# Optimization experiments

Measured on AMD Instinct MI355X. Metric: run time of the kernel, lower is better.

Reference implementation:

```python
import jax, jax.numpy as jnp
import numpy as np

N, E, IN_DIM, HID, G, NCLS, LAYERS = 200000, 1200000, 128, 64, 1024, 6, 3
BN_EPS = 1e-5


def _bn(x, g, b, m, v):
    # eval-mode BatchNorm1d with running stats
    return (x - m) * jax.lax.rsqrt(v + BN_EPS) * g + b


def setup_inputs() -> dict:
    key = jax.random.key(0)
    ks = jax.random.split(key, 24)
    s = 0.05
    d = {
        "x": jax.random.normal(ks[0], (N, IN_DIM), jnp.float32),
        "edge_index": jax.random.randint(ks[1], (2, E), 0, N, dtype=jnp.int32),
        "batch": jnp.sort(jax.random.randint(ks[2], (N,), 0, G, dtype=jnp.int32)),
        # input embedding + input BN
        "emb_w": jax.random.normal(ks[3], (IN_DIM, HID), jnp.float32) * s,
        "emb_b": jnp.zeros((HID,), jnp.float32),
        "ibn_g": jnp.ones((HID,), jnp.float32),
        "ibn_b": jnp.zeros((HID,), jnp.float32),
        "ibn_m": jax.random.normal(ks[4], (HID,), jnp.float32) * 0.1,
        "ibn_v": jax.random.uniform(ks[5], (HID,), jnp.float32, 0.5, 1.5),
        # stacked per-layer GIN MLP params [LAYERS, ...]
        "fc1_w": jax.random.normal(ks[6], (LAYERS, HID, HID), jnp.float32) * s,
        "fc1_b": jnp.zeros((LAYERS, HID), jnp.float32),
        "mbn_g": jnp.ones((LAYERS, HID), jnp.float32),
        "mbn_b": jnp.zeros((LAYERS, HID), jnp.float32),
        "mbn_m": jax.random.normal(ks[7], (LAYERS, HID), jnp.float32) * 0.1,
        "mbn_v": jax.random.uniform(ks[8], (LAYERS, HID), jnp.float32, 0.5, 1.5),
        "fc2_w": jax.random.normal(ks[9], (LAYERS, HID, HID), jnp.float32) * s,
        "fc2_b": jnp.zeros((LAYERS, HID), jnp.float32),
        # stacked per-layer outer BN params
        "obn_g": jnp.ones((LAYERS, HID), jnp.float32),
        "obn_b": jnp.zeros((LAYERS, HID), jnp.float32),
        "obn_m": jax.random.normal(ks[10], (LAYERS, HID), jnp.float32) * 0.1,
        "obn_v": jax.random.uniform(ks[11], (LAYERS, HID), jnp.float32, 0.5, 1.5),
        # classifier head
        "cls1_w": jax.random.normal(ks[12], (HID, HID // 2), jnp.float32) * s,
        "cls1_b": jnp.zeros((HID // 2,), jnp.float32),
        "cls2_w": jax.random.normal(ks[13], (HID // 2, NCLS), jnp.float32) * s,
        "cls2_b": jnp.zeros((NCLS,), jnp.float32),
    }
    return d


def reference(x, edge_index, batch,
              emb_w, emb_b, ibn_g, ibn_b, ibn_m, ibn_v,
              fc1_w, fc1_b, mbn_g, mbn_b, mbn_m, mbn_v, fc2_w, fc2_b,
              obn_g, obn_b, obn_m, obn_v,
              cls1_w, cls1_b, cls2_w, cls2_b):
    n = x.shape[0]
    src, dst = edge_index[0], edge_index[1]

    # input embed -> BN -> relu (dropout = identity in eval)
    h = jnp.dot(x, emb_w) + emb_b
    h = jax.nn.relu(_bn(h, ibn_g, ibn_b, ibn_m, ibn_v))

    for i in range(LAYERS):
        # GINConv (eps=0): aggregate neighbors via scatter-add, then MLP
        agg = jax.ops.segment_sum(h[src], dst, num_segments=n)
        z = h + agg
        z = jnp.dot(z, fc1_w[i]) + fc1_b[i]
        z = jax.nn.relu(_bn(z, mbn_g[i], mbn_b[i], mbn_m[i], mbn_v[i]))
        z = jnp.dot(z, fc2_w[i]) + fc2_b[i]
        # outer BN + relu
        h = jax.nn.relu(_bn(z, obn_g[i], obn_b[i], obn_m[i], obn_v[i]))

    # global mean pool per graph
    sums = jax.ops.segment_sum(h, batch, num_segments=G)
    cnts = jax.ops.segment_sum(jnp.ones((n,), h.dtype), batch, num_segments=G)
    pooled = sums / jnp.maximum(cnts, 1.0)[:, None]

    # classifier
    out = jax.nn.relu(jnp.dot(pooled, cls1_w) + cls1_b)
    out = jnp.dot(out, cls2_w) + cls2_b
    return out
```

## Files before the change

### kernel.cpp

```cpp
#include <hip/hip_runtime.h>
#include <hip/hip_bf16.h>

#define N_NODES 200000
#define N_EDGES 1200000
#define IN_DIM  128
#define HID     64
#define NGRAPH  1024
#define NCLS    6
#define BN_EPS  1e-5f

#define TILE_N   64
#define ZS       68
#define ECAP     1024

#define SCAN_CHUNK 1024
#define NBLK_SCAN ((N_NODES + SCAN_CHUNK - 1) / SCAN_CHUNK)

#define NBKT   128
#define BRANGE 1568
#define BCAP   12288
#define EPB    4096
#define NB_BIN ((N_EDGES + EPB - 1) / EPB)

#define SWZ(s) ((s) ^ (((s) >> 4) & 3))

typedef short bf16x8 __attribute__((ext_vector_type(8)));
typedef float f32x4  __attribute__((ext_vector_type(4)));
#define MFMA16(a,b,c) __builtin_amdgcn_mfma_f32_16x16x32_bf16((a),(b),(c),0,0,0)

template<bool V> struct BoolC { static constexpr bool value = V; };

__device__ __forceinline__ unsigned short f2bf(float f) {
    union { __hip_bfloat16 h; unsigned short u; } v; v.h = __float2bfloat16(f); return v.u;
}
__device__ __forceinline__ float bfbits2f(unsigned short u) {
    union { unsigned int i; float f; } v; v.i = ((unsigned int)u) << 16; return v.f;
}
__device__ __forceinline__ void cvt4(const f32x4& x, uint2& hi, uint2& lo) {
    const unsigned short h0 = f2bf(x[0]), h1 = f2bf(x[1]), h2 = f2bf(x[2]), h3 = f2bf(x[3]);
    hi.x = (unsigned)h0 | ((unsigned)h1 << 16);
    hi.y = (unsigned)h2 | ((unsigned)h3 << 16);
    const unsigned short l0 = f2bf(x[0] - bfbits2f(h0)), l1 = f2bf(x[1] - bfbits2f(h1));
    const unsigned short l2 = f2bf(x[2] - bfbits2f(h2)), l3 = f2bf(x[3] - bfbits2f(h3));
    lo.x = (unsigned)l0 | ((unsigned)l1 << 16);
    lo.y = (unsigned)l2 | ((unsigned)l3 << 16);
}

__global__ __launch_bounds__(256) void setup_kernel(
    const float* __restrict__ emb_w, unsigned short* __restrict__ wpe,
    const float* __restrict__ fc1, const float* __restrict__ fc2,
    unsigned short* __restrict__ wpf,
    const int* __restrict__ batch, int* __restrict__ goffs,
    int* __restrict__ gcnt)
{
    const int b = blockIdx.x, t = threadIdx.x;
    if (b < 64) {
        const int idx = b * 256 + t;
        const int j = idx & 7, l = (idx >> 3) & 63;
        const int plane = (idx >> 9) & 1, s = (idx >> 10) & 3, ct = (idx >> 12) & 3;
        const int n = ct * 16 + (l & 15);
        const int k = s * 32 + (l >> 4) * 8 + j;
        const float f = emb_w[k * 64 + n];
        const unsigned short hb = f2bf(f);
        wpe[idx] = plane ? f2bf(f - bfbits2f(hb)) : hb;
    } else if (b < 256) {
        const int idx = (b - 64) * 256 + t;
        const int j = idx & 7, l = (idx >> 3) & 63;
        const int plane = (idx >> 9) & 1, s = (idx >> 10) & 1, ct = (idx >> 11) & 3;
        const int g = (idx >> 13) & 1, layer = idx >> 14;
        const int n = ct * 16 + (l & 15);
        const int k = s * 32 + (l >> 4) * 8 + j;
        const float* W = g ? fc2 : fc1;
        const float f = W[(layer * 64 + k) * 64 + n];
        const unsigned short hb = f2bf(f);
        wpf[idx] = plane ? f2bf(f - bfbits2f(hb)) : hb;
    } else {
        if (b == 256 && t < NBKT) gcnt[t] = 0;
        const int g = (b - 256) * 256 + t;
        if (g > NGRAPH) return;
        if (g == NGRAPH) { goffs[NGRAPH] = N_NODES; return; }
        int lo = 0, hi = N_NODES;
        while (lo < hi) {
            const int mid = (lo + hi) >> 1;
            if (batch[mid] < g) lo = mid + 1; else hi = mid;
        }
        goffs[g] = lo;
    }
}

__global__ __launch_bounds__(256) void bin_kernel(
    const int* __restrict__ src, const int* __restrict__ dst,
    int* __restrict__ gcnt, unsigned* __restrict__ ebin)
{
    __shared__ int hist[NBKT];
    __shared__ int basis[NBKT];
    const int t = threadIdx.x;
    const int base = blockIdx.x * EPB;
    if (t < NBKT) hist[t] = 0;
    __syncthreads();
    int sv[16], dv[16];
    #pragma unroll
    for (int i = 0; i < 16; i++) {
        const int e = base + t + i * 256;
        if (e < N_EDGES) {
            sv[i] = __builtin_nontemporal_load(&src[e]);
            dv[i] = __builtin_nontemporal_load(&dst[e]);
            atomicAdd(&hist[dv[i] / BRANGE], 1);
        } else { sv[i] = -1; dv[i] = -1; }
    }
    __syncthreads();
    if (t < NBKT) { basis[t] = atomicAdd(&gcnt[t], hist[t]); hist[t] = 0; }
    __syncthreads();
    #pragma unroll
    for (int i = 0; i < 16; i++) {
        if (dv[i] >= 0) {
            const int bb = dv[i] / BRANGE;
            const int dl = dv[i] - bb * BRANGE;
            const int pos = basis[bb] + atomicAdd(&hist[bb], 1);
            __builtin_nontemporal_store(
                (unsigned)sv[i] | ((unsigned)dl << 18),
                &ebin[(size_t)bb * BCAP + pos]);
        }
    }
}

__global__ __launch_bounds__(512) void bindeg_kernel(
    const int* __restrict__ gcnt, const unsigned* __restrict__ ebin,
    int* __restrict__ deg)
{
    __shared__ int hist[BRANGE];
    const int b = blockIdx.x, t = threadIdx.x;
    for (int i = t; i < BRANGE; i += 512) hist[i] = 0;
    __syncthreads();
    const int cnt = gcnt[b];
    const int r0 = b * BRANGE;
    const unsigned* __restrict__ eb = ebin + (size_t)b * BCAP;
    for (int i = t; i < cnt; i += 512) {
        const unsigned e = __builtin_nontemporal_load(&eb[i]);
        atomicAdd(&hist[e >> 18], 1);
    }
    __syncthreads();
    for (int i = t; i < BRANGE; i += 512)
        if (r0 + i < N_NODES) deg[r0 + i] = hist[i];
}

__global__ __launch_bounds__(512) void binscatter_kernel(
    const int* __restrict__ gcnt, const unsigned* __restrict__ ebin,
    const int* __restrict__ offs, int* __restrict__ csr_src)
{
    __shared__ int cur[BRANGE];
    const int b = blockIdx.x, t = threadIdx.x;
    const int r0 = b * BRANGE;
    const int lim = (r0 + BRANGE <= N_NODES) ? BRANGE : (N_NODES - r0);
    for (int i = t; i < lim; i += 512) cur[i] = offs[r0 + i];
    __syncthreads();
    const int cnt = gcnt[b];
    const unsigned* __restrict__ eb = ebin + (size_t)b * BCAP;
    for (int i = t; i < cnt; i += 512) {
        const unsigned e = __builtin_nontemporal_load(&eb[i]);
        const int pos = atomicAdd(&cur[e >> 18], 1);
        csr_src[pos] = (int)(e & 0x3FFFFu);
    }
}

__global__ __launch_bounds__(256) void scan_sum_kernel(
    const int* __restrict__ deg, int* __restrict__ bsum)
{
    __shared__ int sd[256];
    const int b = blockIdx.x, t = threadIdx.x;
    const int base = b * SCAN_CHUNK;
    int s = 0;
    #pragma unroll
    for (int i = 0; i < SCAN_CHUNK / 256; i++) {
        const int idx = base + t + i * 256;
        s += (idx < N_NODES) ? deg[idx] : 0;
    }
    sd[t] = s; __syncthreads();
    for (int off = 128; off > 0; off >>= 1) {
        if (t < off) sd[t] += sd[t + off];
        __syncthreads();
    }
    if (t == 0) bsum[b] = sd[0];
}

__global__ __launch_bounds__(256) void scan_block_kernel(
    const int* __restrict__ bsum, int* __restrict__ boff, int* __restrict__ offs)
{
    __shared__ int sd[256];
    const int t = threadIdx.x;
    const int v = (t < NBLK_SCAN) ? bsum[t] : 0;
    sd[t] = v; __syncthreads();
    for (int off = 1; off < 256; off <<= 1) {
        const int u = (t >= off) ? sd[t - off] : 0;
        __syncthreads();
        sd[t] += u;
        __syncthreads();
    }
    if (t < NBLK_SCAN) boff[t] = sd[t] - v;
    if (t == 0) offs[N_NODES] = N_EDGES;
}

__global__ __launch_bounds__(256) void scan_scatter_kernel(
    const int* __restrict__ deg, const int* __restrict__ boff, int* __restrict__ offs)
{
    __shared__ int sd[256];
    const int b = blockIdx.x, t = threadIdx.x;
    const int base = b * SCAN_CHUNK + t * 4;
    int d0 = 0, d1 = 0, d2 = 0, d3 = 0;
    if (base + 0 < N_NODES) d0 = deg[base + 0];
    if (base + 1 < N_NODES) d1 = deg[base + 1];
    if (base + 2 < N_NODES) d2 = deg[base + 2];
    if (base + 3 < N_NODES) d3 = deg[base + 3];
    const int ts = d0 + d1 + d2 + d3;
    sd[t] = ts; __syncthreads();
    for (int off = 1; off < 256; off <<= 1) {
        const int u = (t >= off) ? sd[t - off] : 0;
        __syncthreads();
        sd[t] += u;
        __syncthreads();
    }
    const int excl = sd[t] - ts + boff[b];
    if (base + 0 < N_NODES) offs[base + 0] = excl;
    if (base + 1 < N_NODES) offs[base + 1] = excl + d0;
    if (base + 2 < N_NODES) offs[base + 2] = excl + d0 + d1;
    if (base + 3 < N_NODES) offs[base + 3] = excl + d0 + d1 + d2;
}

__global__ __launch_bounds__(256) void pool_kernel(
    const float* __restrict__ h, const int* __restrict__ goffs,
    float* __restrict__ pooled, float* __restrict__ cnt)
{
    __shared__ f32x4 red[4][16];
    const int g = blockIdx.x, t = threadIdx.x;
    const int s = goffs[g], e = goffs[g + 1];
    const int grp = t >> 4;
    const int q = t & 15;
    f32x4 acc = {0.f, 0.f, 0.f, 0.f};
    for (int n = s + grp; n < e; n += 16) {
        const f32x4 v = __builtin_nontemporal_load(
            (const f32x4*)(h + (size_t)n * HID + q * 4));
        acc += v;
    }
    #pragma unroll
    for (int off = 16; off <= 32; off <<= 1) {
        acc[0] += __shfl_xor(acc[0], off, 64);
        acc[1] += __shfl_xor(acc[1], off, 64);
        acc[2] += __shfl_xor(acc[2], off, 64);
        acc[3] += __shfl_xor(acc[3], off, 64);
    }
    const int wv = t >> 6, lane = t & 63;
    if (lane < 16) red[wv][lane] = acc;
    __syncthreads();
    if (t < 16) {
        f32x4 a = red[0][t] + red[1][t] + red[2][t] + red[3][t];
        *(f32x4*)(pooled + (size_t)g * HID + t * 4) = a;
    }
    if (t == 0) cnt[g] = (float)(e - s);
}

__global__ __launch_bounds__(256) void embed_kernel(
    const float* __restrict__ x, const unsigned short* __restrict__ wpe,
    const float* __restrict__ bias,
    const float* __restrict__ bn_g, const float* __restrict__ bn_b,
    const float* __restrict__ bn_m, const float* __restrict__ bn_v,
    float* __restrict__ h)
{
    __shared__ __align__(16) float Ush[8192];
    __shared__ float BNs[128];
    short* Abuf = (short*)Ush;
    float* Ztmp = Ush;
    const int t = threadIdx.x, lane = t & 63, w = t >> 6;
    const int base = blockIdx.x * TILE_N;

    if (t < 64) {
        const float s = bn_g[t] * rsqrtf(bn_v[t] + BN_EPS);
        BNs[t] = s;
        BNs[64 + t] = bias[t] * s + bn_b[t] - bn_m[t] * s;
    }
    #pragma unroll
    for (int i = 0; i < 8; i++) {
        const int idx = t + i * 256;
        const int n = idx >> 5, k4 = idx & 31;
        const f32x4 v = __builtin_nontemporal_load(
            (const f32x4*)(x + (size_t)(base + n) * IN_DIM + k4 * 4));
        uint2 hi, lo; cvt4(v, hi, lo);
        const int s = k4 >> 3, lc = (n & 15) + 16 * ((k4 >> 1) & 3);
        const int half = k4 & 1, wm = n >> 4;
        const int sl0 = ((wm * 4 + s) * 2 + 0) * 64 + lc;
        const int sl1 = ((wm * 4 + s) * 2 + 1) * 64 + lc;
        *(uint2*)&Abuf[SWZ(sl0) * 8 + half * 4] = hi;
        *(uint2*)&Abuf[SWZ(sl1) * 8 + half * 4] = lo;
    }
    __syncthreads();

    const bf16x8* A = (const bf16x8*)Abuf;
    const bf16x8* B = (const bf16x8*)wpe;
    bf16x8 ah[4], al[4];
    #pragma unroll
    for (int s = 0; s < 4; s++) {
        ah[s] = A[SWZ(((w * 4 + s) * 2 + 0) * 64 + lane)];
        al[s] = A[SWZ(((w * 4 + s) * 2 + 1) * 64 + lane)];
    }
    __syncthreads();
    const int q = lane >> 4, c = lane & 15;
    #pragma unroll
    for (int ct = 0; ct < 4; ct++) {
        f32x4 acc = {0.f, 0.f, 0.f, 0.f};
        #pragma unroll
        for (int s = 0; s < 4; s++) {
            const bf16x8 bh = B[(ct << 9) + (s << 7) + lane];
            const bf16x8 bl = B[(ct << 9) + (s << 7) + 64 + lane];
            acc = MFMA16(ah[s], bh, acc);
            acc = MFMA16(ah[s], bl, acc);
            acc = MFMA16(al[s], bh, acc);
        }
        const int n = ct * 16 + c;
        const float sc = BNs[n], sh = BNs[64 + n];
        #pragma unroll
        for (int r = 0; r < 4; r++)
            Ztmp[(w * 16 + q * 4 + r) * ZS + n] = fmaxf(acc[r] * sc + sh, 0.f);
    }
    __syncthreads();
    #pragma unroll
    for (int i = 0; i < 4; i++) {
        const int idx = t + i * 256, n = idx >> 4, k4 = idx & 15;
        *(f32x4*)(h + (size_t)(base + n) * HID + k4 * 4) =
            *(const f32x4*)(&Ztmp[n * ZS + k4 * 4]);
    }
}

__global__ __launch_bounds__(256, 7) void agg_mlp_kernel(
    const float* __restrict__ hin, float* __restrict__ hout,
    const int* __restrict__ offs, const int* __restrict__ csr,
    const unsigned short* __restrict__ wp1, const unsigned short* __restrict__ wp2,
    const float* __restrict__ b1, const float* __restrict__ g1,
    const float* __restrict__ bb1, const float* __restrict__ m1, const float* __restrict__ v1,
    const float* __restrict__ b2, const float* __restrict__ g2,
    const float* __restrict__ bb2, const float* __restrict__ m2, const float* __restrict__ v2)
{
    __shared__ __align__(16) float Ush[TILE_N * ZS];
    __shared__ int   OF[TILE_N + 1];
    __shared__ int   EIDX[ECAP];
    __shared__ float BNs[256];
    short* Abuf = (short*)Ush;
    float* Ztmp = Ush;
    const int t = threadIdx.x, lane = t & 63, w = t >> 6;
    const int sub = lane >> 4, cq = lane & 15;
    const int base = blockIdx.x * TILE_N;

    if (t < 64) {
        const float sa = g1[t] * rsqrtf(v1[t] + BN_EPS);
        BNs[t] = sa; BNs[64 + t] = b1[t] * sa + bb1[t] - m1[t] * sa;
        const float sb = g2[t] * rsqrtf(v2[t] + BN_EPS);
        BNs[128 + t] = sb; BNs[192 + t] = b2[t] * sb + bb2[t] - m2[t] * sb;
    }
    if (t <= TILE_N) OF[t] = offs[base + t];
    const int segStart = offs[base];
    const int segEnd   = offs[base + TILE_N];
    for (int i = t; i < segEnd - segStart; i += 256)
        if (i < ECAP) EIDX[i] = csr[segStart + i];
    __syncthreads();

    const float* __restrict__ hc = hin + cq * 4;
    const bool allLds = (segEnd - segStart) <= ECAP;

    auto gather_pass = [&](auto ldsTag) {
        constexpr bool LDSONLY = decltype(ldsTag)::value;
        #pragma unroll
        for (int pp = 0; pp < 2; pp++) {
            const int mlA = (pp * 2 + 0) * 4 + sub;
            const int mlB = (pp * 2 + 1) * 4 + sub;
            const int nlA = w * 16 + mlA, nlB = w * 16 + mlB;
            int eA = OF[nlA]; const int eA1 = OF[nlA + 1];
            int eB = OF[nlB]; const int eB1 = OF[nlB + 1];
            const int eAm = (eA1 - 1 > segStart) ? eA1 - 1 : segStart;
            const int eBm = (eB1 - 1 > segStart) ? eB1 - 1 : segStart;
            f32x4 accA = *(const f32x4*)(hin + (size_t)(base + nlA) * HID + cq * 4);
            f32x4 accB = *(const f32x4*)(hin + (size_t)(base + nlB) * HID + cq * 4);
            while (eA < eA1 || eB < eB1) {
                int ia[4], ib[4];
                #pragma unroll
                for (int k = 0; k < 4; k++) {
                    const int ea = (eA + k < eAm) ? eA + k : eAm;
                    const int eb = (eB + k < eBm) ? eB + k : eBm;
                    const int la = ea - segStart, lb = eb - segStart;
                    if (LDSONLY) {
                        ia[k] = EIDX[la];
                        ib[k] = EIDX[lb];
                    } else {
                        ia[k] = (la < ECAP) ? EIDX[la] : csr[ea];
                        ib[k] = (lb < ECAP) ? EIDX[lb] : csr[eb];
                    }
                }
                f32x4 va[4], vb[4];
                #pragma unroll
                for (int k = 0; k < 4; k++) {
                    va[k] = *(const f32x4*)(hc + (size_t)ia[k] * HID);
                    vb[k] = *(const f32x4*)(hc + (size_t)ib[k] * HID);
                }
                #pragma unroll
                for (int k = 0; k < 4; k++) {
                    const float ma = (eA + k < eA1) ? 1.f : 0.f;
                    const float mb = (eB + k < eB1) ? 1.f : 0.f;
                    accA += va[k] * ma;
                    accB += vb[k] * mb;
                }
                eA += 4; eB += 4;
            }
            {
                uint2 hi, lo; cvt4(accA, hi, lo);
                const int s = cq >> 3, lc = mlA + 16 * ((cq >> 1) & 3), half = cq & 1;
                const int sl0 = ((w * 2 + s) * 2 + 0) * 64 + lc;
                const int sl1 = ((w * 2 + s) * 2 + 1) * 64 + lc;
                *(uint2*)&Abuf[SWZ(sl0) * 8 + half * 4] = hi;
                *(uint2*)&Abuf[SWZ(sl1) * 8 + half * 4] = lo;
            }
            {
                uint2 hi, lo; cvt4(accB, hi, lo);
                const int s = cq >> 3, lc = mlB + 16 * ((cq >> 1) & 3), half = cq & 1;
                const int sl0 = ((w * 2 + s) * 2 + 0) * 64 + lc;
                const int sl1 = ((w * 2 + s) * 2 + 1) * 64 + lc;
                *(uint2*)&Abuf[SWZ(sl0) * 8 + half * 4] = hi;
                *(uint2*)&Abuf[SWZ(sl1) * 8 + half * 4] = lo;
            }
        }
    };
    if (allLds) gather_pass(BoolC<true>{});
    else        gather_pass(BoolC<false>{});
    __syncthreads();

    const bf16x8* A = (const bf16x8*)Abuf;
    const int q = lane >> 4, c = lane & 15;

    {
        const bf16x8 a0h = A[SWZ(((w * 2 + 0) * 2 + 0) * 64 + lane)];
        const bf16x8 a0l = A[SWZ(((w * 2 + 0) * 2 + 1) * 64 + lane)];
        const bf16x8 a1h = A[SWZ(((w * 2 + 1) * 2 + 0) * 64 + lane)];
        const bf16x8 a1l = A[SWZ(((w * 2 + 1) * 2 + 1) * 64 + lane)];
        __syncthreads();
        const bf16x8* B = (const bf16x8*)wp1;
        #pragma unroll
        for (int ct = 0; ct < 4; ct++) {
            const bf16x8 b0h = B[(ct << 8) + lane];
            const bf16x8 b0l = B[(ct << 8) + 64 + lane];
            const bf16x8 b1h_ = B[(ct << 8) + 128 + lane];
            const bf16x8 b1l_ = B[(ct << 8) + 192 + lane];
            f32x4 acc = {0.f, 0.f, 0.f, 0.f};
            acc = MFMA16(a0h, b0h, acc);
            acc = MFMA16(a0h, b0l, acc);
            acc = MFMA16(a0l, b0h, acc);
            acc = MFMA16(a1h, b1h_, acc);
            acc = MFMA16(a1h, b1l_, acc);
            acc = MFMA16(a1l, b1h_, acc);
            const int n = ct * 16 + c;
            const float sc = BNs[n], sh = BNs[64 + n];
            #pragma unroll
            for (int r = 0; r < 4; r++)
                Ztmp[(w * 16 + q * 4 + r) * ZS + n] = fmaxf(acc[r] * sc + sh, 0.f);
        }
    }
    __syncthreads();

    {
        const int m = t >> 2;
        f32x4 vv[4];
        #pragma unroll
        for (int d = 0; d < 4; d++) {
            const int k4 = (t & 3) * 4 + d;
            vv[d] = *(const f32x4*)(&Ztmp[m * ZS + k4 * 4]);
        }
        __syncthreads();
        #pragma unroll
        for (int d = 0; d < 4; d++) {
            const int k4 = (t & 3) * 4 + d;
            uint2 hi, lo; cvt4(vv[d], hi, lo);
            const int s = k4 >> 3, lc = (m & 15) + 16 * ((k4 >> 1) & 3);
            const int half = k4 & 1, wm = m >> 4;
            const int sl0 = ((wm * 2 + s) * 2 + 0) * 64 + lc;
            const int sl1 = ((wm * 2 + s) * 2 + 1) * 64 + lc;
            *(uint2*)&Abuf[SWZ(sl0) * 8 + half * 4] = hi;
            *(uint2*)&Abuf[SWZ(sl1) * 8 + half * 4] = lo;
        }
    }
    __syncthreads();

    {
        const bf16x8 a0h = A[SWZ(((w * 2 + 0) * 2 + 0) * 64 + lane)];
        const bf16x8 a0l = A[SWZ(((w * 2 + 0) * 2 + 1) * 64 + lane)];
        const bf16x8 a1h = A[SWZ(((w * 2 + 1) * 2 + 0) * 64 + lane)];
        const bf16x8 a1l = A[SWZ(((w * 2 + 1) * 2 + 1) * 64 + lane)];
        __syncthreads();
        const bf16x8* B = (const bf16x8*)wp2;
        #pragma unroll
        for (int ct = 0; ct < 4; ct++) {
            const bf16x8 b0h = B[(ct << 8) + lane];
            const bf16x8 b0l = B[(ct << 8) + 64 + lane];
            const bf16x8 b1h_ = B[(ct << 8) + 128 + lane];
            const bf16x8 b1l_ = B[(ct << 8) + 192 + lane];
            f32x4 acc = {0.f, 0.f, 0.f, 0.f};
            acc = MFMA16(a0h, b0h, acc);
            acc = MFMA16(a0h, b0l, acc);
            acc = MFMA16(a0l, b0h, acc);
            acc = MFMA16(a1h, b1h_, acc);
            acc = MFMA16(a1h, b1l_, acc);
            acc = MFMA16(a1l, b1h_, acc);
            const int n = ct * 16 + c;
            const float sc = BNs[128 + n], sh = BNs[192 + n];
            #pragma unroll
            for (int r = 0; r < 4; r++)
                Ztmp[(w * 16 + q * 4 + r) * ZS + n] = fmaxf(acc[r] * sc + sh, 0.f);
        }
    }
    __syncthreads();

    #pragma unroll
    for (int i = 0; i < 4; i++) {
        const int idx = t + i * 256, n = idx >> 4, k4 = idx & 15;
        *(f32x4*)(hout + (size_t)(base + n) * HID + k4 * 4) =
            *(const f32x4*)(&Ztmp[n * ZS + k4 * 4]);
    }
}

__global__ __launch_bounds__(64) void cls_kernel(
    const float* __restrict__ pooled, const float* __restrict__ cnt,
    const float* __restrict__ w1, const float* __restrict__ b1,
    const float* __restrict__ w2, const float* __restrict__ b2,
    float* __restrict__ out)
{
    const int g = blockIdx.x;
    const int lane = threadIdx.x;
    const float c = cnt[g];
    const float p = pooled[(size_t)g * HID + lane] / fmaxf(c, 1.f);
    float acc = (lane < 32) ? b1[lane] : 0.f;
    #pragma unroll
    for (int k = 0; k < 64; k++) {
        const float pk = __shfl(p, k, 64);
        if (lane < 32) acc += pk * w1[k * 32 + lane];
    }
    const float hmid = fmaxf(acc, 0.f);
    float acc2 = (lane < NCLS) ? b2[lane] : 0.f;
    #pragma unroll
    for (int k = 0; k < 32; k++) {
        const float hk = __shfl(hmid, k, 64);
        if (lane < NCLS) acc2 += hk * w2[k * NCLS + lane];
    }
    if (lane < NCLS) out[(size_t)g * NCLS + lane] = acc2;
}

extern "C" void kernel_launch(void* const* d_in, const int* in_sizes, int n_in,
                              void* d_out, int out_size, void* d_ws, size_t ws_size,
                              hipStream_t stream) {
    const float* x     = (const float*)d_in[0];
    const int*   ei    = (const int*)d_in[1];
    const int*   batch = (const int*)d_in[2];
    const float* emb_w = (const float*)d_in[3];
    const float* emb_b = (const float*)d_in[4];
    const float* ibn_g = (const float*)d_in[5];
    const float* ibn_b = (const float*)d_in[6];
    const float* ibn_m = (const float*)d_in[7];
    const float* ibn_v = (const float*)d_in[8];
    const float* fc1_w = (const float*)d_in[9];
    const float* fc1_b = (const float*)d_in[10];
    const float* mbn_g = (const float*)d_in[11];
    const float* mbn_b = (const float*)d_in[12];
    const float* mbn_m = (const float*)d_in[13];
    const float* mbn_v = (const float*)d_in[14];
    const float* fc2_w = (const float*)d_in[15];
    const float* fc2_b = (const float*)d_in[16];
    const float* obn_g = (const float*)d_in[17];
    const float* obn_b = (const float*)d_in[18];
    const float* obn_m = (const float*)d_in[19];
    const float* obn_v = (const float*)d_in[20];
    const float* cls1w = (const float*)d_in[21];
    const float* cls1b = (const float*)d_in[22];
    const float* cls2w = (const float*)d_in[23];
    const float* cls2b = (const float*)d_in[24];

    float* h0     = (float*)d_ws;
    float* h1     = h0 + (size_t)N_NODES * HID;
    float* pooled = h1 + (size_t)N_NODES * HID;
    float* cnt    = pooled + NGRAPH * HID;
    int*   deg    = (int*)(cnt + NGRAPH);
    int*   offs   = deg + N_NODES;
    int*   bsum   = offs + (N_NODES + 1);
    int*   boff   = bsum + NBLK_SCAN;
    int*   csr    = boff + NBLK_SCAN;
    unsigned short* wpe = (unsigned short*)(csr + N_EDGES);
    unsigned short* wpf = wpe + 16384;
    int*   goffs  = (int*)(wpf + 49152);
    int*   gcnt   = goffs + (NGRAPH + 1);
    unsigned* ebin = (unsigned*)h0;

    const int* src = ei;
    const int* dst = ei + N_EDGES;

    setup_kernel<<<261, 256, 0, stream>>>(emb_w, wpe, fc1_w, fc2_w, wpf,
                                          batch, goffs, gcnt);

    bin_kernel<<<NB_BIN, 256, 0, stream>>>(src, dst, gcnt, ebin);
    bindeg_kernel<<<NBKT, 512, 0, stream>>>(gcnt, ebin, deg);
    scan_sum_kernel<<<NBLK_SCAN, 256, 0, stream>>>(deg, bsum);
    scan_block_kernel<<<1, 256, 0, stream>>>(bsum, boff, offs);
    scan_scatter_kernel<<<NBLK_SCAN, 256, 0, stream>>>(deg, boff, offs);
    binscatter_kernel<<<NBKT, 512, 0, stream>>>(gcnt, ebin, offs, csr);

    const int gemm_blocks = N_NODES / TILE_N;
    embed_kernel<<<gemm_blocks, 256, 0, stream>>>(x, wpe, emb_b,
                                                  ibn_g, ibn_b, ibn_m, ibn_v, h0);

    const float* hin = h0;
    float* hout = h1;
    for (int i = 0; i < 3; i++) {
        agg_mlp_kernel<<<gemm_blocks, 256, 0, stream>>>(
            hin, hout, offs, csr,
            wpf + (size_t)(i * 2 + 0) * 8192, wpf + (size_t)(i * 2 + 1) * 8192,
            fc1_b + i * HID, mbn_g + i * HID, mbn_b + i * HID, mbn_m + i * HID, mbn_v + i * HID,
            fc2_b + i * HID, obn_g + i * HID, obn_b + i * HID, obn_m + i * HID, obn_v + i * HID);
        const float* tmp = hin; hin = hout; hout = (float*)tmp;
    }

    pool_kernel<<<NGRAPH, 256, 0, stream>>>(h1, goffs, pooled, cnt);

    cls_kernel<<<NGRAPH, 64, 0, stream>>>(pooled, cnt, cls1w, cls1b, cls2w, cls2b,
                                          (float*)d_out);
}
```

Baseline: 496.2 us.

## Fuse CSR offset scan into bin-degree kernel and mean-pool into last GIN layer

Replaces the degree histogram plus three-kernel global scan with one kernel. Each bucket block builds its local histogram, scans the bucket counts to get its base, and writes CSR offsets directly. The last GIN layer now accumulates per-graph sums with atomics instead of writing h, which removes the separate pool kernel and one full h write and read. It also relaxes launch bounds occupancy from 7 to 6 and adds a memset. The trade-off is atomic contention on pooled and nondeterministic float summation order.

After: 465.7 us. 6.1% less time.

```diff
diff --git a/kernel.cpp b/kernel.cpp
--- a/kernel.cpp
+++ b/kernel.cpp
@@ -12,9 +12,6 @@
 #define TILE_N   64
 #define ZS       68
 #define ECAP     1024
-
-#define SCAN_CHUNK 1024
-#define NBLK_SCAN ((N_NODES + SCAN_CHUNK - 1) / SCAN_CHUNK)
 
 #define NBKT   128
 #define BRANGE 1568
@@ -124,24 +121,52 @@
     }
 }
 
-__global__ __launch_bounds__(512) void bindeg_kernel(
+__global__ __launch_bounds__(512) void binoffs_kernel(
     const int* __restrict__ gcnt, const unsigned* __restrict__ ebin,
-    int* __restrict__ deg)
+    int* __restrict__ offs)
 {
     __shared__ int hist[BRANGE];
+    __shared__ int bscan[NBKT];
+    __shared__ int pscan[512];
     const int b = blockIdx.x, t = threadIdx.x;
     for (int i = t; i < BRANGE; i += 512) hist[i] = 0;
+    if (t < NBKT) bscan[t] = gcnt[t];
     __syncthreads();
     const int cnt = gcnt[b];
-    const int r0 = b * BRANGE;
     const unsigned* __restrict__ eb = ebin + (size_t)b * BCAP;
     for (int i = t; i < cnt; i += 512) {
         const unsigned e = __builtin_nontemporal_load(&eb[i]);
         atomicAdd(&hist[e >> 18], 1);
     }
     __syncthreads();
-    for (int i = t; i < BRANGE; i += 512)
-        if (r0 + i < N_NODES) deg[r0 + i] = hist[i];
+    for (int off = 1; off < NBKT; off <<= 1) {
+        const int u = (t >= off && t < NBKT) ? bscan[t - off] : 0;
+        __syncthreads();
+        if (t < NBKT) bscan[t] += u;
+        __syncthreads();
+    }
+    const int bucketBase = (b == 0) ? 0 : bscan[b - 1];
+    const int i0 = t * 4;
+    const int h0v = (i0 + 0 < BRANGE) ? hist[i0 + 0] : 0;
+    const int h1v = (i0 + 1 < BRANGE) ? hist[i0 + 1] : 0;
+    const int h2v = (i0 + 2 < BRANGE) ? hist[i0 + 2] : 0;
+    const int h3v = (i0 + 3 < BRANGE) ? hist[i0 + 3] : 0;
+    const int ts = h0v + h1v + h2v + h3v;
+    pscan[t] = ts;
+    __syncthreads();
+    for (int off = 1; off < 512; off <<= 1) {
+        const int u = (t >= off) ? pscan[t - off] : 0;
+        __syncthreads();
+        pscan[t] += u;
+        __syncthreads();
+    }
+    const int excl = pscan[t] - ts + bucketBase;
+    const int r0 = b * BRANGE;
+    if (i0 + 0 < BRANGE && r0 + i0 + 0 < N_NODES) offs[r0 + i0 + 0] = excl;
+    if (i0 + 1 < BRANGE && r0 + i0 + 1 < N_NODES) offs[r0 + i0 + 1] = excl + h0v;
+    if (i0 + 2 < BRANGE && r0 + i0 + 2 < N_NODES) offs[r0 + i0 + 2] = excl + h0v + h1v;
+    if (i0 + 3 < BRANGE && r0 + i0 + 3 < N_NODES) offs[r0 + i0 + 3] = excl + h0v + h1v + h2v;
+    if (b == NBKT - 1 && t == 0) offs[N_NODES] = N_EDGES;
 }
 
 __global__ __launch_bounds__(512) void binscatter_kernel(
@@ -161,101 +186,6 @@
         const int pos = atomicAdd(&cur[e >> 18], 1);
         csr_src[pos] = (int)(e & 0x3FFFFu);
     }
-}
-
-__global__ __launch_bounds__(256) void scan_sum_kernel(
-    const int* __restrict__ deg, int* __restrict__ bsum)
-{
-    __shared__ int sd[256];
-    const int b = blockIdx.x, t = threadIdx.x;
-    const int base = b * SCAN_CHUNK;
-    int s = 0;
-    #pragma unroll
-    for (int i = 0; i < SCAN_CHUNK / 256; i++) {
-        const int idx = base + t + i * 256;
-        s += (idx < N_NODES) ? deg[idx] : 0;
-    }
-    sd[t] = s; __syncthreads();
-    for (int off = 128; off > 0; off >>= 1) {
-        if (t < off) sd[t] += sd[t + off];
-        __syncthreads();
-    }
-    if (t == 0) bsum[b] = sd[0];
-}
-
-__global__ __launch_bounds__(256) void scan_block_kernel(
-    const int* __restrict__ bsum, int* __restrict__ boff, int* __restrict__ offs)
-{
-    __shared__ int sd[256];
-    const int t = threadIdx.x;
-    const int v = (t < NBLK_SCAN) ? bsum[t] : 0;
-    sd[t] = v; __syncthreads();
-    for (int off = 1; off < 256; off <<= 1) {
-        const int u = (t >= off) ? sd[t - off] : 0;
-        __syncthreads();
-        sd[t] += u;
-        __syncthreads();
-    }
-    if (t < NBLK_SCAN) boff[t] = sd[t] - v;
-    if (t == 0) offs[N_NODES] = N_EDGES;
-}
-
-__global__ __launch_bounds__(256) void scan_scatter_kernel(
-    const int* __restrict__ deg, const int* __restrict__ boff, int* __restrict__ offs)
-{
-    __shared__ int sd[256];
-    const int b = blockIdx.x, t = threadIdx.x;
-    const int base = b * SCAN_CHUNK + t * 4;
-    int d0 = 0, d1 = 0, d2 = 0, d3 = 0;
-    if (base + 0 < N_NODES) d0 = deg[base + 0];
-    if (base + 1 < N_NODES) d1 = deg[base + 1];
-    if (base + 2 < N_NODES) d2 = deg[base + 2];
-    if (base + 3 < N_NODES) d3 = deg[base + 3];
-    const int ts = d0 + d1 + d2 + d3;
-    sd[t] = ts; __syncthreads();
-    for (int off = 1; off < 256; off <<= 1) {
-        const int u = (t >= off) ? sd[t - off] : 0;
-        __syncthreads();
-        sd[t] += u;
-        __syncthreads();
-    }
-    const int excl = sd[t] - ts + boff[b];
-    if (base + 0 < N_NODES) offs[base + 0] = excl;
-    if (base + 1 < N_NODES) offs[base + 1] = excl + d0;
-    if (base + 2 < N_NODES) offs[base + 2] = excl + d0 + d1;
-    if (base + 3 < N_NODES) offs[base + 3] = excl + d0 + d1 + d2;
-}
-
-__global__ __launch_bounds__(256) void pool_kernel(
-    const float* __restrict__ h, const int* __restrict__ goffs,
-    float* __restrict__ pooled, float* __restrict__ cnt)
-{
-    __shared__ f32x4 red[4][16];
-    const int g = blockIdx.x, t = threadIdx.x;
-    const int s = goffs[g], e = goffs[g + 1];
-    const int grp = t >> 4;
-    const int q = t & 15;
-    f32x4 acc = {0.f, 0.f, 0.f, 0.f};
-    for (int n = s + grp; n < e; n += 16) {
-        const f32x4 v = __builtin_nontemporal_load(
-            (const f32x4*)(h + (size_t)n * HID + q * 4));
-        acc += v;
-    }
-    #pragma unroll
-    for (int off = 16; off <= 32; off <<= 1) {
-        acc[0] += __shfl_xor(acc[0], off, 64);
-        acc[1] += __shfl_xor(acc[1], off, 64);
-        acc[2] += __shfl_xor(acc[2], off, 64);
-        acc[3] += __shfl_xor(acc[3], off, 64);
-    }
-    const int wv = t >> 6, lane = t & 63;
-    if (lane < 16) red[wv][lane] = acc;
-    __syncthreads();
-    if (t < 16) {
-        f32x4 a = red[0][t] + red[1][t] + red[2][t] + red[3][t];
-        *(f32x4*)(pooled + (size_t)g * HID + t * 4) = a;
-    }
-    if (t == 0) cnt[g] = (float)(e - s);
 }
 
 __global__ __launch_bounds__(256) void embed_kernel(
@@ -329,9 +259,11 @@
     }
 }
 
-__global__ __launch_bounds__(256, 7) void agg_mlp_kernel(
+template<bool POOL>
+__global__ __launch_bounds__(256, 6) void agg_mlp_kernel(
     const float* __restrict__ hin, float* __restrict__ hout,
     const int* __restrict__ offs, const int* __restrict__ csr,
+    const int* __restrict__ batch, float* __restrict__ pooled,
     const unsigned short* __restrict__ wp1, const unsigned short* __restrict__ wp2,
     const float* __restrict__ b1, const float* __restrict__ g1,
     const float* __restrict__ bb1, const float* __restrict__ m1, const float* __restrict__ v1,
@@ -342,6 +274,7 @@
     __shared__ int   OF[TILE_N + 1];
     __shared__ int   EIDX[ECAP];
     __shared__ float BNs[256];
+    __shared__ int   GID[TILE_N];
     short* Abuf = (short*)Ush;
     float* Ztmp = Ush;
     const int t = threadIdx.x, lane = t & 63, w = t >> 6;
@@ -353,6 +286,7 @@
         BNs[t] = sa; BNs[64 + t] = b1[t] * sa + bb1[t] - m1[t] * sa;
         const float sb = g2[t] * rsqrtf(v2[t] + BN_EPS);
         BNs[128 + t] = sb; BNs[192 + t] = b2[t] * sb + bb2[t] - m2[t] * sb;
+        if (POOL) GID[t] = batch[base + t];
     }
     if (t <= TILE_N) OF[t] = offs[base + t];
     const int segStart = offs[base];
@@ -513,23 +447,40 @@
     }
     __syncthreads();
 
-    #pragma unroll
-    for (int i = 0; i < 4; i++) {
-        const int idx = t + i * 256, n = idx >> 4, k4 = idx & 15;
-        *(f32x4*)(hout + (size_t)(base + n) * HID + k4 * 4) =
-            *(const f32x4*)(&Ztmp[n * ZS + k4 * 4]);
+    if (POOL) {
+        const int cc = t & 63, rg = t >> 6;
+        float run = 0.f;
+        int cur = GID[rg * 16];
+        #pragma unroll
+        for (int r = 0; r < 16; r++) {
+            const int row = rg * 16 + r;
+            const int g = GID[row];
+            if (g != cur) {
+                atomicAdd(&pooled[(size_t)cur * HID + cc], run);
+                run = 0.f; cur = g;
+            }
+            run += Ztmp[row * ZS + cc];
+        }
+        atomicAdd(&pooled[(size_t)cur * HID + cc], run);
+    } else {
+        #pragma unroll
+        for (int i = 0; i < 4; i++) {
+            const int idx = t + i * 256, n = idx >> 4, k4 = idx & 15;
+            *(f32x4*)(hout + (size_t)(base + n) * HID + k4 * 4) =
+                *(const f32x4*)(&Ztmp[n * ZS + k4 * 4]);
+        }
     }
 }
 
 __global__ __launch_bounds__(64) void cls_kernel(
-    const float* __restrict__ pooled, const float* __restrict__ cnt,
+    const float* __restrict__ pooled, const int* __restrict__ goffs,
     const float* __restrict__ w1, const float* __restrict__ b1,
     const float* __restrict__ w2, const float* __restrict__ b2,
     float* __restrict__ out)
 {
     const int g = blockIdx.x;
     const int lane = threadIdx.x;
-    const float c = cnt[g];
+    const float c = (float)(goffs[g + 1] - goffs[g]);
     const float p = pooled[(size_t)g * HID + lane] / fmaxf(c, 1.f);
     float acc = (lane < 32) ? b1[lane] : 0.f;
     #pragma unroll
@@ -583,8 +534,8 @@
     int*   deg    = (int*)(cnt + NGRAPH);
     int*   offs   = deg + N_NODES;
     int*   bsum   = offs + (N_NODES + 1);
-    int*   boff   = bsum + NBLK_SCAN;
-    int*   csr    = boff + NBLK_SCAN;
+    int*   boff   = bsum + 256;
+    int*   csr    = boff + 256;
     unsigned short* wpe = (unsigned short*)(csr + N_EDGES);
     unsigned short* wpf = wpe + 16384;
     int*   goffs  = (int*)(wpf + 49152);
@@ -596,12 +547,10 @@
 
     setup_kernel<<<261, 256, 0, stream>>>(emb_w, wpe, fc1_w, fc2_w, wpf,
                                           batch, goffs, gcnt);
+    hipMemsetAsync(pooled, 0, (size_t)NGRAPH * HID * sizeof(float), stream);
 
     bin_kernel<<<NB_BIN, 256, 0, stream>>>(src, dst, gcnt, ebin);
-    bindeg_kernel<<<NBKT, 512, 0, stream>>>(gcnt, ebin, deg);
-    scan_sum_kernel<<<NBLK_SCAN, 256, 0, stream>>>(deg, bsum);
-    scan_block_kernel<<<1, 256, 0, stream>>>(bsum, boff, offs);
-    scan_scatter_kernel<<<NBLK_SCAN, 256, 0, stream>>>(deg, boff, offs);
+    binoffs_kernel<<<NBKT, 512, 0, stream>>>(gcnt, ebin, offs);
     binscatter_kernel<<<NBKT, 512, 0, stream>>>(gcnt, ebin, offs, csr);
 
     const int gemm_blocks = N_NODES / TILE_N;
@@ -611,16 +560,21 @@
     const float* hin = h0;
     float* hout = h1;
     for (int i = 0; i < 3; i++) {
-        agg_mlp_kernel<<<gemm_blocks, 256, 0, stream>>>(
-            hin, hout, offs, csr,
-            wpf + (size_t)(i * 2 + 0) * 8192, wpf + (size_t)(i * 2 + 1) * 8192,
-            fc1_b + i * HID, mbn_g + i * HID, mbn_b + i * HID, mbn_m + i * HID, mbn_v + i * HID,
-            fc2_b + i * HID, obn_g + i * HID, obn_b + i * HID, obn_m + i * HID, obn_v + i * HID);
+        if (i < 2)
+            agg_mlp_kernel<false><<<gemm_blocks, 256, 0, stream>>>(
+                hin, hout, offs, csr, batch, pooled,
+                wpf + (size_t)(i * 2 + 0) * 8192, wpf + (size_t)(i * 2 + 1) * 8192,
+                fc1_b + i * HID, mbn_g + i * HID, mbn_b + i * HID, mbn_m + i * HID, mbn_v + i * HID,
+                fc2_b + i * HID, obn_g + i * HID, obn_b + i * HID, obn_m + i * HID, obn_v + i * HID);
+        else
+            agg_mlp_kernel<true><<<gemm_blocks, 256, 0, stream>>>(
+                hin, hout, offs, csr, batch, pooled,
+                wpf + (size_t)(i * 2 + 0) * 8192, wpf + (size_t)(i * 2 + 1) * 8192,
+                fc1_b + i * HID, mbn_g + i * HID, mbn_b + i * HID, mbn_m + i * HID, mbn_v + i * HID,
+                fc2_b + i * HID, obn_g + i * HID, obn_b + i * HID, obn_m + i * HID, obn_v + i * HID);
         const float* tmp = hin; hin = hout; hout = (float*)tmp;
     }
 
-    pool_kernel<<<NGRAPH, 256, 0, stream>>>(h1, goffs, pooled, cnt);
-
-    cls_kernel<<<NGRAPH, 64, 0, stream>>>(pooled, cnt, cls1w, cls1b, cls2w, cls2b,
+    cls_kernel<<<NGRAPH, 64, 0, stream>>>(pooled, goffs, cls1w, cls1b, cls2w, cls2b,
                                           (float*)d_out);
 }
```
